# Kernel optimization log

Measured on AMD Instinct MI355X. Metric: run time of the kernel, lower is better.

## Reference

```python
import jax, jax.numpy as jnp
import numpy as np

BINS = 8
EPS = 1e-12  # torch F.normalize default eps


def _pairwise_scores(matf):
    # torch: input1[a,b]=matf[b]; transpose(0,1)->matf[a]; transpose(-2,-1)->matf[a]^T [M,F]
    # matmul with input1[a,b]=matf[b] -> scores[a,b] = matf[a]^T @ matf[b], shape [M,M]
    bs, F, M = matf.shape
    s = jnp.einsum('afm,bfn->abmn', matf, matf)  # [bs, bs, M, M]
    return s.reshape(bs * bs, M * M)


def _histc_rows(x, bins):
    # torch.histc semantics with min=max=0: range = [row.min(), row.max()],
    # values == max land in the last bin.
    mn = jnp.min(x, axis=1, keepdims=True)
    mx = jnp.max(x, axis=1, keepdims=True)
    denom = jnp.where(mx > mn, mx - mn, jnp.ones_like(mx))
    idx = jnp.clip(jnp.floor((x - mn) / denom * bins).astype(jnp.int32), 0, bins - 1)
    nbs = x.shape[0]
    flat = (idx + (jnp.arange(nbs, dtype=jnp.int32) * bins)[:, None]).ravel()
    h = jnp.zeros(nbs * bins, dtype=x.dtype).at[flat].add(1.0)
    return h.reshape(nbs, bins)


def _l2_normalize(h):
    n = jnp.linalg.norm(h, axis=-1, keepdims=True)
    return h / jnp.maximum(n, EPS)


def setup_inputs() -> dict:
    key = jax.random.key(0)
    k1, k2 = jax.random.split(key)
    bs, F, M = 64, 256, 128
    matf1 = jax.random.normal(k1, (bs, F, M), dtype=jnp.float32)
    matf2 = jax.random.normal(k2, (bs, F, M), dtype=jnp.float32)
    return {"matf1": matf1, "matf2": matf2}


def reference(matf1, matf2):
    # scores are .detach()ed in the original; stop_gradient for faithfulness
    scores1 = jax.lax.stop_gradient(_pairwise_scores(matf1))  # [nbs, M*M]
    scores2 = jax.lax.stop_gradient(_pairwise_scores(matf2))
    h1 = _l2_normalize(_histc_rows(scores1, BINS))  # [nbs, 8]
    h2 = _l2_normalize(_histc_rows(scores2, BINS))
    return jnp.concatenate([h1, h2], axis=-1)  # [nbs, 16]
```

## Files before the change

kernel.cpp:

```cpp
#include <hip/hip_runtime.h>
#include <math.h>

#define BS 64
#define F  256
#define M  128
#define MF (M * F)
#define NT2 528

typedef unsigned short u16;
typedef _Float16 f16x8 __attribute__((ext_vector_type(8)));
typedef float    f32x16 __attribute__((ext_vector_type(16)));

typedef const __attribute__((address_space(1))) void gas_t;
typedef __attribute__((address_space(3))) void las_t;

__global__ __launch_bounds__(256) void convert_f16_kernel(
    const float* __restrict__ m1, const float* __restrict__ m2,
    u16* __restrict__ hT)
{
    __shared__ float tile[64 * M];
    const int mat = blockIdx.x >> 6;
    const int b   = blockIdx.x & 63;
    const int f0  = blockIdx.y * 64;
    const float* src = (mat == 0 ? m1 : m2) + (size_t)b * MF + (size_t)f0 * M;
    const int tid = threadIdx.x;

    const float4* g = (const float4*)src;
    float4* s = (float4*)tile;
    #pragma unroll
    for (int i = 0; i < 8; ++i)
        s[tid + i * 256] = g[tid + i * 256];
    __syncthreads();

    const size_t obase = ((size_t)(mat * BS + b) * 32 + (f0 >> 3)) * 1024;
    #pragma unroll
    for (int it = 0; it < 4; ++it) {
        const int idx = it * 256 + tid;
        const int f8l = idx >> 7;
        const int m   = idx & 127;
        u16 hh[8] __attribute__((aligned(16)));
        #pragma unroll
        for (int j = 0; j < 8; ++j) {
            const float x = tile[(f8l * 8 + j) * M + m];
            const _Float16 h = (_Float16)x;
            hh[j] = __builtin_bit_cast(u16, h);
        }
        *(uint4*)&hT[obase + (size_t)idx * 8] = *(const uint4*)hh;
    }
}


#define GLOAD(S, BUF) {                                                       \
    const u16* g0 = srow + (S) * 4096 + j0 * 512 + lane * 8;                  \
    const u16* g1 = srow + (S) * 4096 + j1 * 512 + lane * 8;                  \
    __builtin_amdgcn_global_load_lds((gas_t*)g0,                              \
        (las_t*)&lds[ldst0 + (BUF)], 16, 0, 0);                               \
    __builtin_amdgcn_global_load_lds((gas_t*)g1,                              \
        (las_t*)&lds[ldst1 + (BUF)], 16, 0, 0);                               \
}

#define MFMA_SLICE(BUF) {                                                     \
    __builtin_amdgcn_s_setprio(1);                                            \
    _Pragma("unroll")                                                         \
    for (int kk = 0; kk < 2; ++kk) {                                          \
        const int ab = ra * 8192 + (BUF) + kk * 2048 + aoffb;                 \
        const int bb = rb * 8192 + (BUF) + kk * 2048 + boffb;                 \
        const f16x8 a0 = *(const f16x8*)&lds[ab];                             \
        const f16x8 a1 = *(const f16x8*)&lds[ab + 256];                       \
        const f16x8 b0 = *(const f16x8*)&lds[bb];                             \
        const f16x8 b1 = *(const f16x8*)&lds[bb + 256];                       \
        acc[0][0] = __builtin_amdgcn_mfma_f32_32x32x16_f16(a0, b0, acc[0][0], 0, 0, 0); \
        acc[0][1] = __builtin_amdgcn_mfma_f32_32x32x16_f16(a0, b1, acc[0][1], 0, 0, 0); \
        acc[1][0] = __builtin_amdgcn_mfma_f32_32x32x16_f16(a1, b0, acc[1][0], 0, 0, 0); \
        acc[1][1] = __builtin_amdgcn_mfma_f32_32x32x16_f16(a1, b1, acc[1][1], 0, 0, 0); \
    }                                                                         \
    __builtin_amdgcn_s_setprio(0);                                            \
}

__global__ __launch_bounds__(1024, 4) void gram_hist_mfma(
    const u16* __restrict__ hT, float* __restrict__ out)
{
    __shared__ u16 lds[4 * 2 * 4096];
    __shared__ float smin[16], smax[16];
    __shared__ int hist[4][8];

    const int tid  = threadIdx.x;
    const int lane = tid & 63;
    const int w    = tid >> 6;

    if (tid < 32) hist[tid >> 3][tid & 7] = 0;

    const int bid = blockIdx.x;
    const int xcd = bid & 7;
    const int mat = xcd >> 2;
    int p = (xcd & 3) * 132 + (bid >> 3);
    int ta = 0;
    { int cnt = 32; while (p >= cnt) { p -= cnt; ++ta; cnt = 32 - ta; } }
    const int tb = ta + p;

    const int m  = w >> 2;
    const int q  = w & 3;
    const int qr = q >> 1;
    const int qc = q & 1;
    const int l31   = lane & 31;
    const int lhalf = lane >> 5;

    const int k0  = w * 2;
    const int r_s = k0 >> 3;
    const int rowsel = (r_s < 2) ? (2 * ta + r_s) : (2 * tb + (r_s - 2));
    const u16* srow = hT + (size_t)(mat * BS + rowsel) * MF;
    const int j0 = k0 & 7, j1 = (k0 + 1) & 7;
    const int ldst0 = r_s * 8192 + j0 * 512;
    const int ldst1 = r_s * 8192 + j1 * 512;

    const int ra = m >> 1;
    const int rb = 2 + (m & 1);
    const int aoffb = lhalf * 1024 + qr * 512 + l31 * 8;
    const int boffb = lhalf * 1024 + qc * 512 + l31 * 8;

    f32x16 acc[2][2];
    #pragma unroll
    for (int t = 0; t < 2; ++t)
        #pragma unroll
        for (int u = 0; u < 2; ++u)
            #pragma unroll
            for (int r = 0; r < 16; ++r) acc[t][u][r] = 0.0f;

    GLOAD(0, 0);
    __syncthreads();

    #pragma unroll
    for (int s = 0; s < 8; ++s) {
        const int cur = (s & 1) * 4096;
        const int alt = cur ^ 4096;
        if (s < 7) GLOAD(s + 1, alt);
        MFMA_SLICE(cur);
        __syncthreads();
    }

    float vmin = acc[0][0][0], vmax = vmin;
    #pragma unroll
    for (int t = 0; t < 2; ++t)
        #pragma unroll
        for (int u = 0; u < 2; ++u)
            #pragma unroll
            for (int r = 0; r < 16; ++r) {
                vmin = fminf(vmin, acc[t][u][r]);
                vmax = fmaxf(vmax, acc[t][u][r]);
            }
    #pragma unroll
    for (int off = 1; off < 64; off <<= 1) {
        vmin = fminf(vmin, __shfl_xor(vmin, off, 64));
        vmax = fmaxf(vmax, __shfl_xor(vmax, off, 64));
    }
    if (lane == 0) { smin[w] = vmin; smax[w] = vmax; }
    __syncthreads();
    const int m4 = m * 4;
    const float pmn = fminf(fminf(smin[m4], smin[m4 + 1]),
                            fminf(smin[m4 + 2], smin[m4 + 3]));
    const float pmx = fmaxf(fmaxf(smax[m4], smax[m4 + 1]),
                            fmaxf(smax[m4 + 2], smax[m4 + 3]));
    const float denom = (pmx > pmn) ? (pmx - pmn) : 1.0f;
    const float scale = 8.0f / denom;
    const float bias  = -pmn * scale;

    unsigned w0 = 0, w1 = 0;
    #pragma unroll
    for (int t = 0; t < 2; ++t)
        #pragma unroll
        for (int u = 0; u < 2; ++u)
            #pragma unroll
            for (int r = 0; r < 16; ++r) {
                const float tv = fmaf(acc[t][u][r], scale, bias);
                int k = (int)tv;
                k = k > 7 ? 7 : k;
                const unsigned inc = 1u << ((k & 3) * 8);
                if (k < 4) w0 += inc; else w1 += inc;
            }
    unsigned e0 = (w0 & 0xFFu)         | (((w0 >> 8)  & 0xFFu) << 16);
    unsigned e1 = ((w0 >> 16) & 0xFFu) | (((w0 >> 24) & 0xFFu) << 16);
    unsigned e2 = (w1 & 0xFFu)         | (((w1 >> 8)  & 0xFFu) << 16);
    unsigned e3 = ((w1 >> 16) & 0xFFu) | (((w1 >> 24) & 0xFFu) << 16);
    #pragma unroll
    for (int off = 32; off > 0; off >>= 1) {
        e0 += __shfl_down(e0, off, 64);
        e1 += __shfl_down(e1, off, 64);
        e2 += __shfl_down(e2, off, 64);
        e3 += __shfl_down(e3, off, 64);
    }
    if (lane == 0) {
        atomicAdd(&hist[m][0], (int)(e0 & 0xFFFFu)); atomicAdd(&hist[m][1], (int)(e0 >> 16));
        atomicAdd(&hist[m][2], (int)(e1 & 0xFFFFu)); atomicAdd(&hist[m][3], (int)(e1 >> 16));
        atomicAdd(&hist[m][4], (int)(e2 & 0xFFFFu)); atomicAdd(&hist[m][5], (int)(e2 >> 16));
        atomicAdd(&hist[m][6], (int)(e3 & 0xFFFFu)); atomicAdd(&hist[m][7], (int)(e3 >> 16));
    }
    __syncthreads();

    if (q == 0 && lane < 8) {
        float ss = 0.0f;
        #pragma unroll
        for (int k = 0; k < 8; ++k) {
            const float cc = (float)hist[m][k];
            ss += cc * cc;
        }
        const float nrm = fmaxf(sqrtf(ss), 1e-12f);
        const float v = (float)hist[m][lane] / nrm;
        const int A = 2 * ta + (m >> 1);
        const int B = 2 * tb + (m & 1);
        out[((size_t)A * BS + B) * 16 + mat * 8 + lane] = v;
        if (A != B)
            out[((size_t)B * BS + A) * 16 + mat * 8 + lane] = v;
    }
}

extern "C" void kernel_launch(void* const* d_in, const int* in_sizes, int n_in,
                              void* d_out, int out_size, void* d_ws, size_t ws_size,
                              hipStream_t stream) {
    const float* m1 = (const float*)d_in[0];
    const float* m2 = (const float*)d_in[1];
    float* out = (float*)d_out;

    u16* hT = (u16*)d_ws;

    convert_f16_kernel<<<dim3(128, 4), 256, 0, stream>>>(m1, m2, hT);
    gram_hist_mfma<<<2 * NT2, 1024, 0, stream>>>(hT, out);
}
```

Baseline: 133.8 us.

## Use one 256-thread block per matrix pair with register-staged double buffering

The gram/histogram kernel now gives each workgroup a single (a,b) pair with 4 waves, instead of a 2x2 tile of pairs with 16 waves. Operands are staged through registers into double-buffered LDS rather than via direct global-to-LDS loads. This gives more, smaller blocks for better scheduling and smaller LDS per block. In exchange, each operand row is reloaded once per pair it appears in rather than shared across a 2x2 tile.

New measurement: 119.3 us. -10.8%, faster.

```diff
diff --git a/kernel.cpp b/kernel.cpp
--- a/kernel.cpp
+++ b/kernel.cpp
@@ -5,14 +5,11 @@
 #define F  256
 #define M  128
 #define MF (M * F)
-#define NT2 528
+#define NPAIR 2080
 
 typedef unsigned short u16;
 typedef _Float16 f16x8 __attribute__((ext_vector_type(8)));
 typedef float    f32x16 __attribute__((ext_vector_type(16)));
-
-typedef const __attribute__((address_space(1))) void gas_t;
-typedef __attribute__((address_space(3))) void las_t;
 
 __global__ __launch_bounds__(256) void convert_f16_kernel(
     const float* __restrict__ m1, const float* __restrict__ m2,
@@ -50,73 +47,38 @@
 }
 
 
-#define GLOAD(S, BUF) {                                                       \
-    const u16* g0 = srow + (S) * 4096 + j0 * 512 + lane * 8;                  \
-    const u16* g1 = srow + (S) * 4096 + j1 * 512 + lane * 8;                  \
-    __builtin_amdgcn_global_load_lds((gas_t*)g0,                              \
-        (las_t*)&lds[ldst0 + (BUF)], 16, 0, 0);                               \
-    __builtin_amdgcn_global_load_lds((gas_t*)g1,                              \
-        (las_t*)&lds[ldst1 + (BUF)], 16, 0, 0);                               \
-}
-
-#define MFMA_SLICE(BUF) {                                                     \
-    __builtin_amdgcn_s_setprio(1);                                            \
-    _Pragma("unroll")                                                         \
-    for (int kk = 0; kk < 2; ++kk) {                                          \
-        const int ab = ra * 8192 + (BUF) + kk * 2048 + aoffb;                 \
-        const int bb = rb * 8192 + (BUF) + kk * 2048 + boffb;                 \
-        const f16x8 a0 = *(const f16x8*)&lds[ab];                             \
-        const f16x8 a1 = *(const f16x8*)&lds[ab + 256];                       \
-        const f16x8 b0 = *(const f16x8*)&lds[bb];                             \
-        const f16x8 b1 = *(const f16x8*)&lds[bb + 256];                       \
-        acc[0][0] = __builtin_amdgcn_mfma_f32_32x32x16_f16(a0, b0, acc[0][0], 0, 0, 0); \
-        acc[0][1] = __builtin_amdgcn_mfma_f32_32x32x16_f16(a0, b1, acc[0][1], 0, 0, 0); \
-        acc[1][0] = __builtin_amdgcn_mfma_f32_32x32x16_f16(a1, b0, acc[1][0], 0, 0, 0); \
-        acc[1][1] = __builtin_amdgcn_mfma_f32_32x32x16_f16(a1, b1, acc[1][1], 0, 0, 0); \
-    }                                                                         \
-    __builtin_amdgcn_s_setprio(0);                                            \
-}
-
-__global__ __launch_bounds__(1024, 4) void gram_hist_mfma(
+__global__ __launch_bounds__(256, 4) void gram_hist_mfma(
     const u16* __restrict__ hT, float* __restrict__ out)
 {
-    __shared__ u16 lds[4 * 2 * 4096];
-    __shared__ float smin[16], smax[16];
-    __shared__ int hist[4][8];
+    __shared__ u16 lds[2 * 8192];
+    __shared__ float smin[4], smax[4];
+    __shared__ int hist[8];
 
     const int tid  = threadIdx.x;
     const int lane = tid & 63;
     const int w    = tid >> 6;
 
-    if (tid < 32) hist[tid >> 3][tid & 7] = 0;
+    if (tid < 8) hist[tid] = 0;
 
     const int bid = blockIdx.x;
     const int xcd = bid & 7;
     const int mat = xcd >> 2;
-    int p = (xcd & 3) * 132 + (bid >> 3);
-    int ta = 0;
-    { int cnt = 32; while (p >= cnt) { p -= cnt; ++ta; cnt = 32 - ta; } }
-    const int tb = ta + p;
-
-    const int m  = w >> 2;
-    const int q  = w & 3;
-    const int qr = q >> 1;
-    const int qc = q & 1;
+    int p = (xcd & 3) * 520 + (bid >> 3);
+    int a = 0;
+    { int cnt = 64; while (p >= cnt) { p -= cnt; ++a; --cnt; } }
+    const int b = a + p;
+
+    const int qr = w >> 1;
+    const int qc = w & 1;
     const int l31   = lane & 31;
     const int lhalf = lane >> 5;
 
-    const int k0  = w * 2;
-    const int r_s = k0 >> 3;
-    const int rowsel = (r_s < 2) ? (2 * ta + r_s) : (2 * tb + (r_s - 2));
-    const u16* srow = hT + (size_t)(mat * BS + rowsel) * MF;
-    const int j0 = k0 & 7, j1 = (k0 + 1) & 7;
-    const int ldst0 = r_s * 8192 + j0 * 512;
-    const int ldst1 = r_s * 8192 + j1 * 512;
-
-    const int ra = m >> 1;
-    const int rb = 2 + (m & 1);
-    const int aoffb = lhalf * 1024 + qr * 512 + l31 * 8;
-    const int boffb = lhalf * 1024 + qc * 512 + l31 * 8;
+    const u16* pa = hT + (size_t)(mat * BS + a) * MF + tid * 8;
+    const u16* pb = hT + (size_t)(mat * BS + b) * MF + tid * 8;
+    const int dA0 = tid * 8;
+    const int dA1 = 2048 + tid * 8;
+    const int dB0 = 4096 + tid * 8;
+    const int dB1 = 4096 + 2048 + tid * 8;
 
     f32x16 acc[2][2];
     #pragma unroll
@@ -126,15 +88,51 @@
             #pragma unroll
             for (int r = 0; r < 16; ++r) acc[t][u][r] = 0.0f;
 
-    GLOAD(0, 0);
+    uint4 rA0, rA1, rB0, rB1;
+
+    rA0 = *(const uint4*)(pa);
+    rA1 = *(const uint4*)(pa + 2048);
+    rB0 = *(const uint4*)(pb);
+    rB1 = *(const uint4*)(pb + 2048);
+    *(uint4*)&lds[dA0] = rA0;
+    *(uint4*)&lds[dA1] = rA1;
+    *(uint4*)&lds[dB0] = rB0;
+    *(uint4*)&lds[dB1] = rB1;
     __syncthreads();
 
     #pragma unroll
     for (int s = 0; s < 8; ++s) {
-        const int cur = (s & 1) * 4096;
-        const int alt = cur ^ 4096;
-        if (s < 7) GLOAD(s + 1, alt);
-        MFMA_SLICE(cur);
+        const int cur = (s & 1) * 8192;
+        const int alt = cur ^ 8192;
+
+        if (s < 7) {
+            const int koff = (s + 1) * 4096;
+            rA0 = *(const uint4*)(pa + koff);
+            rA1 = *(const uint4*)(pa + koff + 2048);
+            rB0 = *(const uint4*)(pb + koff);
+            rB1 = *(const uint4*)(pb + koff + 2048);
+        }
+
+        #pragma unroll
+        for (int kk = 0; kk < 2; ++kk) {
+            const int kb = cur + kk * 2048 + lhalf * 1024;
+            f16x8 af[2], bf[2];
+            af[0] = *(const f16x8*)&lds[kb + qr * 512 + l31 * 8];
+            af[1] = *(const f16x8*)&lds[kb + qr * 512 + 256 + l31 * 8];
+            bf[0] = *(const f16x8*)&lds[kb + 4096 + qc * 512 + l31 * 8];
+            bf[1] = *(const f16x8*)&lds[kb + 4096 + qc * 512 + 256 + l31 * 8];
+            acc[0][0] = __builtin_amdgcn_mfma_f32_32x32x16_f16(af[0], bf[0], acc[0][0], 0, 0, 0);
+            acc[0][1] = __builtin_amdgcn_mfma_f32_32x32x16_f16(af[0], bf[1], acc[0][1], 0, 0, 0);
+            acc[1][0] = __builtin_amdgcn_mfma_f32_32x32x16_f16(af[1], bf[0], acc[1][0], 0, 0, 0);
+            acc[1][1] = __builtin_amdgcn_mfma_f32_32x32x16_f16(af[1], bf[1], acc[1][1], 0, 0, 0);
+        }
+
+        if (s < 7) {
+            *(uint4*)&lds[alt + dA0] = rA0;
+            *(uint4*)&lds[alt + dA1] = rA1;
+            *(uint4*)&lds[alt + dB0] = rB0;
+            *(uint4*)&lds[alt + dB1] = rB1;
+        }
         __syncthreads();
     }
 
@@ -155,11 +153,8 @@
     }
     if (lane == 0) { smin[w] = vmin; smax[w] = vmax; }
     __syncthreads();
-    const int m4 = m * 4;
-    const float pmn = fminf(fminf(smin[m4], smin[m4 + 1]),
-                            fminf(smin[m4 + 2], smin[m4 + 3]));
-    const float pmx = fmaxf(fmaxf(smax[m4], smax[m4 + 1]),
-                            fmaxf(smax[m4 + 2], smax[m4 + 3]));
+    const float pmn = fminf(fminf(smin[0], smin[1]), fminf(smin[2], smin[3]));
+    const float pmx = fmaxf(fmaxf(smax[0], smax[1]), fmaxf(smax[2], smax[3]));
     const float denom = (pmx > pmn) ? (pmx - pmn) : 1.0f;
     const float scale = 8.0f / denom;
     const float bias  = -pmn * scale;
@@ -189,27 +184,25 @@
         e3 += __shfl_down(e3, off, 64);
     }
     if (lane == 0) {
-        atomicAdd(&hist[m][0], (int)(e0 & 0xFFFFu)); atomicAdd(&hist[m][1], (int)(e0 >> 16));
-        atomicAdd(&hist[m][2], (int)(e1 & 0xFFFFu)); atomicAdd(&hist[m][3], (int)(e1 >> 16));
-        atomicAdd(&hist[m][4], (int)(e2 & 0xFFFFu)); atomicAdd(&hist[m][5], (int)(e2 >> 16));
-        atomicAdd(&hist[m][6], (int)(e3 & 0xFFFFu)); atomicAdd(&hist[m][7], (int)(e3 >> 16));
-    }
-    __syncthreads();
-
-    if (q == 0 && lane < 8) {
+        atomicAdd(&hist[0], (int)(e0 & 0xFFFFu)); atomicAdd(&hist[1], (int)(e0 >> 16));
+        atomicAdd(&hist[2], (int)(e1 & 0xFFFFu)); atomicAdd(&hist[3], (int)(e1 >> 16));
+        atomicAdd(&hist[4], (int)(e2 & 0xFFFFu)); atomicAdd(&hist[5], (int)(e2 >> 16));
+        atomicAdd(&hist[6], (int)(e3 & 0xFFFFu)); atomicAdd(&hist[7], (int)(e3 >> 16));
+    }
+    __syncthreads();
+
+    if (w == 0 && lane < 8) {
         float ss = 0.0f;
         #pragma unroll
         for (int k = 0; k < 8; ++k) {
-            const float cc = (float)hist[m][k];
+            const float cc = (float)hist[k];
             ss += cc * cc;
         }
         const float nrm = fmaxf(sqrtf(ss), 1e-12f);
-        const float v = (float)hist[m][lane] / nrm;
-        const int A = 2 * ta + (m >> 1);
-        const int B = 2 * tb + (m & 1);
-        out[((size_t)A * BS + B) * 16 + mat * 8 + lane] = v;
-        if (A != B)
-            out[((size_t)B * BS + A) * 16 + mat * 8 + lane] = v;
+        const float v = (float)hist[lane] / nrm;
+        out[((size_t)a * BS + b) * 16 + mat * 8 + lane] = v;
+        if (a != b)
+            out[((size_t)b * BS + a) * 16 + mat * 8 + lane] = v;
     }
 }
 
@@ -223,5 +216,5 @@
     u16* hT = (u16*)d_ws;
 
     convert_f16_kernel<<<dim3(128, 4), 256, 0, stream>>>(m1, m2, hT);
-    gram_hist_mfma<<<2 * NT2, 1024, 0, stream>>>(hT, out);
+    gram_hist_mfma<<<2 * NPAIR, 256, 0, stream>>>(hT, out);
 }
```
